# Performance work log

Measured on AMD Instinct MI355X. Metric: run time of the kernel, lower is better.

## Reference

```python
import jax, jax.numpy as jnp
import numpy as np

N_COMPANIES = 2000
HIDDEN = 256
HEADS = 8
LAYERS = 3
IN_DIM = 64
NEG_SLOPE = 0.2  # PyG GATConv default leaky_relu slope


def setup_inputs() -> dict:
    key = jax.random.key(0)
    ks = jax.random.split(key, 32)
    B, E = 64, 64000
    C = HIDDEN // HEADS
    emb_dim = HIDDEN // 4
    def lin(k, fo, fi):
        k1, k2 = jax.random.split(k)
        s = 1.0 / np.sqrt(fi)
        return (jax.random.uniform(k1, (fo, fi), jnp.float32, -s, s),
                jax.random.uniform(k2, (fo,), jnp.float32, -s, s))
    inp = {}
    inp['x'] = jax.random.normal(ks[0], (B, IN_DIM), jnp.float32)
    inp['company_indices'] = jax.random.randint(ks[1], (B,), 0, N_COMPANIES)
    inp['edge_index'] = jax.random.randint(ks[2], (2, E), 0, N_COMPANIES)
    inp['edge_attr'] = jax.random.uniform(ks[3], (E,), jnp.float32)
    inp['W_in'], inp['b_in'] = lin(ks[4], HIDDEN, IN_DIM)
    # stacked GAT params (all layers same shape)
    g = 0.05
    inp['gat_W'] = g * jax.random.normal(ks[5], (LAYERS, HEADS * C, HIDDEN), jnp.float32)
    inp['gat_att_src'] = g * jax.random.normal(ks[6], (LAYERS, HEADS, C), jnp.float32)
    inp['gat_att_dst'] = g * jax.random.normal(ks[7], (LAYERS, HEADS, C), jnp.float32)
    inp['gat_We'] = g * jax.random.normal(ks[8], (LAYERS, HEADS * C, 1), jnp.float32)
    inp['gat_att_edge'] = g * jax.random.normal(ks[9], (LAYERS, HEADS, C), jnp.float32)
    inp['gat_b'] = jnp.zeros((LAYERS, HEADS * C), jnp.float32)
    inp['emb'] = jax.random.normal(ks[10], (N_COMPANIES, emb_dim), jnp.float32)
    inp['W_fuse'], inp['b_fuse'] = lin(ks[11], HIDDEN, HIDDEN + emb_dim)
    inp['W_p1'], inp['b_p1'] = lin(ks[12], HIDDEN // 2, HIDDEN)
    inp['W_p2'], inp['b_p2'] = lin(ks[13], HIDDEN // 4, HIDDEN // 2)
    inp['W_p3'], inp['b_p3'] = lin(ks[14], 1, HIDDEN // 4)
    inp['W_d1'], inp['b_d1'] = lin(ks[15], HIDDEN // 2, HIDDEN)
    inp['W_d2'], inp['b_d2'] = lin(ks[16], HIDDEN // 4, HIDDEN // 2)
    inp['W_d3'], inp['b_d3'] = lin(ks[17], 1, HIDDEN // 4)
    return inp


def _gat_layer(xg, src, dst, ea, W, att_s, att_d, We, att_e, b, N):
    # xg: [N, F] node features; src/dst: [E2] (with self-loops); ea: [E2]
    H, C = att_s.shape
    xp = (xg @ W.T).reshape(N, H, C)
    a_s = jnp.sum(xp * att_s, -1)                       # [N, H]
    a_d = jnp.sum(xp * att_d, -1)                       # [N, H]
    ef = (ea[:, None] @ We.T).reshape(-1, H, C)         # [E2, H, C]
    a_e = jnp.sum(ef * att_e, -1)                       # [E2, H]
    logits = jax.nn.leaky_relu(a_s[src] + a_d[dst] + a_e, NEG_SLOPE)
    m = jax.ops.segment_max(logits, dst, num_segments=N)
    ex = jnp.exp(logits - m[dst])
    denom = jax.ops.segment_sum(ex, dst, num_segments=N)
    alpha = ex / (denom[dst] + 1e-16)                   # per-dst softmax
    out = jax.ops.segment_sum(alpha[:, :, None] * xp[src], dst, num_segments=N)
    return out.reshape(N, H * C) + b


def reference(x, company_indices, edge_index, edge_attr, W_in, b_in,
              gat_W, gat_att_src, gat_att_dst, gat_We, gat_att_edge, gat_b,
              emb, W_fuse, b_fuse, W_p1, b_p1, W_p2, b_p2, W_p3, b_p3,
              W_d1, b_d1, W_d2, b_d2, W_d3, b_d3):
    # eval mode: dropout is identity
    B = x.shape[0]
    N = emb.shape[0]
    h = jax.nn.relu(x @ W_in.T + b_in)                  # [B, hidden]
    # add self loops (PyG default, fill_value='mean' for edge_attr)
    loops = jnp.arange(N, dtype=edge_index.dtype)
    src = jnp.concatenate([edge_index[0], loops])
    dst = jnp.concatenate([edge_index[1], loops])
    ea = jnp.concatenate([edge_attr, jnp.full((N,), edge_attr.mean(), edge_attr.dtype)])

    def per_item(hi):
        g = jnp.broadcast_to(hi, (N, hi.shape[0]))
        for l in range(gat_W.shape[0]):
            g = jax.nn.relu(_gat_layer(g, src, dst, ea, gat_W[l], gat_att_src[l],
                                       gat_att_dst[l], gat_We[l], gat_att_edge[l], gat_b[l], N))
        return g

    gouts = jax.vmap(per_item)(h)                       # [B, N, hidden]
    comp_out = gouts[jnp.arange(B), company_indices]    # [B, hidden]
    comp_emb = emb[company_indices]                     # [B, hidden//4]
    fused = jax.nn.relu(jnp.concatenate([comp_out, comp_emb], -1) @ W_fuse.T + b_fuse)
    p = jax.nn.relu(fused @ W_p1.T + b_p1)
    p = jax.nn.relu(p @ W_p2.T + b_p2)
    price = (p @ W_p3.T + b_p3).squeeze(-1)
    d = jax.nn.relu(fused @ W_d1.T + b_d1)
    d = jax.nn.relu(d @ W_d2.T + b_d2)
    direction = jax.nn.sigmoid((d @ W_d3.T + b_d3)).squeeze(-1)
    return price, direction
```

## Files before the change

### kernel.cpp

```cpp
#include <hip/hip_runtime.h>
#include <math.h>


#define B_ITEMS 64

typedef _Float16 half_t;
typedef _Float16 half8 __attribute__((ext_vector_type(8)));
typedef float f32x4 __attribute__((ext_vector_type(4)));

#define OFF_WIN   0
#define OFF_GAT   16384
#define OFF_FUSE  212992
#define OFF_P1    294912
#define OFF_D1    327680
#define OFF_P2    360448
#define OFF_D2    368640
#define TOT_W     376832

extern "C" __global__ __launch_bounds__(1024) void compress_w(
    const float* __restrict__ W_in, const float* __restrict__ gat_W,
    const float* __restrict__ W_fuse, const float* __restrict__ W_p1,
    const float* __restrict__ W_d1, const float* __restrict__ W_p2,
    const float* __restrict__ W_d2, half_t* __restrict__ ws)
{
    const int e = (blockIdx.x * 1024 + threadIdx.x) * 8;
    const float* src;
    int off;
    if      (e < OFF_GAT)  { src = W_in;   off = e; }
    else if (e < OFF_FUSE) { src = gat_W;  off = e - OFF_GAT; }
    else if (e < OFF_P1)   { src = W_fuse; off = e - OFF_FUSE; }
    else if (e < OFF_D1)   { src = W_p1;   off = e - OFF_P1; }
    else if (e < OFF_P2)   { src = W_d1;   off = e - OFF_D1; }
    else if (e < OFF_D2)   { src = W_p2;   off = e - OFF_P2; }
    else                   { src = W_d2;   off = e - OFF_D2; }
    const float4* s4 = reinterpret_cast<const float4*>(src + off);
    float4 a = s4[0], b = s4[1];
    half8 h = { (_Float16)a.x, (_Float16)a.y, (_Float16)a.z, (_Float16)a.w,
                (_Float16)b.x, (_Float16)b.y, (_Float16)b.z, (_Float16)b.w };
    *reinterpret_cast<half8*>(ws + e) = h;
}

#define LDA 328

template <int KSTEPS>
__device__ __forceinline__ void mfma_tile(const half_t* __restrict__ Wt,
                                          const _Float16* __restrict__ At,
                                          f32x4& c, int kq) {
    const half8* __restrict__ Wp = reinterpret_cast<const half8*>(Wt + kq * 8);
    const _Float16* __restrict__ Ap = At + kq * 8;
#pragma unroll 1
    for (int s = 0; s < KSTEPS; s += 2) {
        half8 b0 = Wp[s * 4];
        half8 a0 = *reinterpret_cast<const half8*>(Ap + s * 32);
        half8 b1 = Wp[s * 4 + 4];
        half8 a1 = *reinterpret_cast<const half8*>(Ap + s * 32 + 32);
        c = __builtin_amdgcn_mfma_f32_16x16x32_f16(a0, b0, c, 0, 0, 0);
        c = __builtin_amdgcn_mfma_f32_16x16x32_f16(a1, b1, c, 0, 0, 0);
    }
}

__device__ __forceinline__ void cwrite(f32x4 c, float bv, _Float16* outbase,
                                       int col, int kq) {
#pragma unroll
    for (int r = 0; r < 4; ++r) {
        float v = fmaxf(c[r] + bv, 0.f);
        outbase[(kq * 4 + r) * LDA + col] = (_Float16)v;
    }
}

extern "C" __global__ __launch_bounds__(1024) void fin_gat_v13(
    const float* __restrict__ x,
    const int* __restrict__ cidx,
    const half_t* __restrict__ ws,
    const float* __restrict__ b_in,
    const float* __restrict__ gat_b,
    const float* __restrict__ emb,
    const float* __restrict__ b_fuse,
    const float* __restrict__ b_p1,
    const float* __restrict__ b_p2,
    const float* __restrict__ W_p3, const float* __restrict__ b_p3,
    const float* __restrict__ b_d1,
    const float* __restrict__ b_d2,
    const float* __restrict__ W_d3, const float* __restrict__ b_d3,
    float* __restrict__ out)
{
    __shared__ _Float16 actA[16 * LDA];
    __shared__ _Float16 actB[16 * LDA];
    __shared__ _Float16 xact[16 * 72];

    const int g = blockIdx.x;
    const int i0 = g * 16;
    const int t = threadIdx.x;
    const int w = t >> 6;
    const int lane = t & 63;
    const int r16 = lane & 15;
    const int kq = lane >> 4;

    {
        const int item = t >> 6, k = t & 63;
        xact[item * 72 + k] = (_Float16)x[(i0 + item) * 64 + k];
        actB[item * LDA + 256 + k] =
            (_Float16)emb[(size_t)cidx[i0 + item] * 64 + k];
    }
    __syncthreads();

    {
        f32x4 c = {0.f, 0.f, 0.f, 0.f};
        mfma_tile<2>(ws + OFF_WIN + (size_t)(w * 16 + r16) * 64,
                     xact + r16 * 72, c, kq);
        cwrite(c, b_in[w * 16 + r16], actA, w * 16 + r16, kq);
    }
    __syncthreads();

    {
        f32x4 c = {0.f, 0.f, 0.f, 0.f};
        mfma_tile<8>(ws + OFF_GAT + (size_t)(w * 16 + r16) * 256,
                     actA + r16 * LDA, c, kq);
        cwrite(c, gat_b[w * 16 + r16], actB, w * 16 + r16, kq);
    }
    __syncthreads();

    {
        f32x4 c = {0.f, 0.f, 0.f, 0.f};
        mfma_tile<8>(ws + OFF_GAT + 65536 + (size_t)(w * 16 + r16) * 256,
                     actB + r16 * LDA, c, kq);
        cwrite(c, gat_b[256 + w * 16 + r16], actA, w * 16 + r16, kq);
    }
    __syncthreads();

    {
        f32x4 c = {0.f, 0.f, 0.f, 0.f};
        mfma_tile<8>(ws + OFF_GAT + 131072 + (size_t)(w * 16 + r16) * 256,
                     actA + r16 * LDA, c, kq);
        cwrite(c, gat_b[512 + w * 16 + r16], actB, w * 16 + r16, kq);
    }
    __syncthreads();

    {
        f32x4 c = {0.f, 0.f, 0.f, 0.f};
        mfma_tile<10>(ws + OFF_FUSE + (size_t)(w * 16 + r16) * 320,
                      actB + r16 * LDA, c, kq);
        cwrite(c, b_fuse[w * 16 + r16], actA, w * 16 + r16, kq);
    }
    __syncthreads();

    {
        f32x4 c = {0.f, 0.f, 0.f, 0.f};
        const half_t* Wt = (w < 8)
            ? ws + OFF_P1 + (size_t)(w * 16 + r16) * 256
            : ws + OFF_D1 + (size_t)((w - 8) * 16 + r16) * 256;
        const float bv = (w < 8) ? b_p1[w * 16 + r16]
                                 : b_d1[(w - 8) * 16 + r16];
        mfma_tile<8>(Wt, actA + r16 * LDA, c, kq);
        cwrite(c, bv, actB, w * 16 + r16, kq);
    }
    __syncthreads();

    if (w < 8) {
        f32x4 c = {0.f, 0.f, 0.f, 0.f};
        const half_t* Wt = (w < 4)
            ? ws + OFF_P2 + (size_t)(w * 16 + r16) * 128
            : ws + OFF_D2 + (size_t)((w - 4) * 16 + r16) * 128;
        const _Float16* At = actB + r16 * LDA + ((w < 4) ? 0 : 128);
        const float bv = (w < 4) ? b_p2[w * 16 + r16]
                                 : b_d2[(w - 4) * 16 + r16];
        mfma_tile<4>(Wt, At, c, kq);
        cwrite(c, bv, actA, w * 16 + r16, kq);
    }
    __syncthreads();

    {
        float v1 = (float)actA[w * LDA + lane] * W_p3[lane];
        float v2 = (float)actA[w * LDA + 64 + lane] * W_d3[lane];
#pragma unroll
        for (int off = 32; off > 0; off >>= 1) {
            v1 += __shfl_down(v1, off, 64);
            v2 += __shfl_down(v2, off, 64);
        }
        if (lane == 0) {
            out[i0 + w] = v1 + b_p3[0];
            const float z = v2 + b_d3[0];
            out[B_ITEMS + i0 + w] = 1.0f / (1.0f + expf(-z));
        }
    }
}

extern "C" void kernel_launch(void* const* d_in, const int* in_sizes, int n_in,
                              void* d_out, int out_size, void* d_ws, size_t ws_size,
                              hipStream_t stream) {
    const float* x      = (const float*)d_in[0];
    const int*   cidx   = (const int*)  d_in[1];
    const float* W_in   = (const float*)d_in[4];
    const float* b_in   = (const float*)d_in[5];
    const float* gat_W  = (const float*)d_in[6];
    const float* gat_b  = (const float*)d_in[11];
    const float* emb    = (const float*)d_in[12];
    const float* W_fuse = (const float*)d_in[13];
    const float* b_fuse = (const float*)d_in[14];
    const float* W_p1   = (const float*)d_in[15];
    const float* b_p1   = (const float*)d_in[16];
    const float* W_p2   = (const float*)d_in[17];
    const float* b_p2   = (const float*)d_in[18];
    const float* W_p3   = (const float*)d_in[19];
    const float* b_p3   = (const float*)d_in[20];
    const float* W_d1   = (const float*)d_in[21];
    const float* b_d1   = (const float*)d_in[22];
    const float* W_d2   = (const float*)d_in[23];
    const float* b_d2   = (const float*)d_in[24];
    const float* W_d3   = (const float*)d_in[25];
    const float* b_d3   = (const float*)d_in[26];

    half_t* ws = (half_t*)d_ws;

    compress_w<<<46, 1024, 0, stream>>>(W_in, gat_W, W_fuse, W_p1, W_d1,
                                        W_p2, W_d2, ws);

    fin_gat_v13<<<4, 1024, 0, stream>>>(
        x, cidx, ws, b_in, gat_b, emb, b_fuse,
        b_p1, b_p2, W_p3, b_p3, b_d1, b_d2, W_d3, b_d3,
        (float*)d_out);
}
```

Baseline: 133.5 us.

## Stream weights into LDS with double-buffered async global_load_lds pipeline

Replaces per-wave direct global loads of fp16 weights inside each MFMA layer with a double-buffered pipeline. Weight chunks are copied asynchronously into XOR-swizzled LDS buffers via global_load_lds, and the next chunk's load overlaps with MFMA consumption of the current one. Biases are hoisted into registers up front. The change targets global-memory latency stalls in the serial layer chain, at the cost of 128KB of LDS, manual waitcnt/barrier management and more synchronisation points.

```diff
diff --git a/kernel.cpp b/kernel.cpp
--- a/kernel.cpp
+++ b/kernel.cpp
@@ -42,33 +42,58 @@
 
 #define LDA 328
 
-template <int KSTEPS>
-__device__ __forceinline__ void mfma_tile(const half_t* __restrict__ Wt,
-                                          const _Float16* __restrict__ At,
-                                          f32x4& c, int kq) {
-    const half8* __restrict__ Wp = reinterpret_cast<const half8*>(Wt + kq * 8);
-    const _Float16* __restrict__ Ap = At + kq * 8;
-#pragma unroll 1
-    for (int s = 0; s < KSTEPS; s += 2) {
-        half8 b0 = Wp[s * 4];
-        half8 a0 = *reinterpret_cast<const half8*>(Ap + s * 32);
-        half8 b1 = Wp[s * 4 + 4];
-        half8 a1 = *reinterpret_cast<const half8*>(Ap + s * 32 + 32);
-        c = __builtin_amdgcn_mfma_f32_16x16x32_f16(a0, b0, c, 0, 0, 0);
-        c = __builtin_amdgcn_mfma_f32_16x16x32_f16(a1, b1, c, 0, 0, 0);
-    }
-}
-
-__device__ __forceinline__ void cwrite(f32x4 c, float bv, _Float16* outbase,
-                                       int col, int kq) {
-#pragma unroll
-    for (int r = 0; r < 4; ++r) {
-        float v = fmaxf(c[r] + bv, 0.f);
-        outbase[(kq * 4 + r) * LDA + col] = (_Float16)v;
-    }
-}
-
-extern "C" __global__ __launch_bounds__(1024) void fin_gat_v13(
+#define WAITV(N)  asm volatile("s_waitcnt vmcnt(" #N ")" ::: "memory")
+#define LGKM0()   asm volatile("s_waitcnt lgkmcnt(0)" ::: "memory")
+#define BARRIER() asm volatile("s_barrier" ::: "memory")
+
+__device__ __forceinline__ void g2l16(const half_t* g, half_t* l) {
+    __builtin_amdgcn_global_load_lds(
+        (const __attribute__((address_space(1))) void*)g,
+        (__attribute__((address_space(3))) void*)l, 16, 0, 0);
+}
+
+template <int LNCH, int NCHUNK, int ROWH, int KOFFC>
+__device__ __forceinline__ void dma_stage(const half_t* __restrict__ base,
+                                          half_t* lbuf, int t) {
+#pragma unroll
+    for (int i = 0; i < NCHUNK / 1024; ++i) {
+        const int n = i * 1024 + t;
+        const int c = n >> LNCH;
+        const int j = (n & ((1 << LNCH) - 1)) ^ (c & 7);
+        g2l16(base + (size_t)c * ROWH + (KOFFC + j) * 8, lbuf + (size_t)n * 8);
+    }
+}
+
+template <int LNCH, int NCHUNK, int ROWH, int KOFFC, int CS>
+__device__ __forceinline__ void dma_split(const half_t* __restrict__ baseA,
+                                          const half_t* __restrict__ baseB,
+                                          half_t* lbuf, int t) {
+#pragma unroll
+    for (int i = 0; i < NCHUNK / 1024; ++i) {
+        const int n = i * 1024 + t;
+        const int c = n >> LNCH;
+        const int j = (n & ((1 << LNCH) - 1)) ^ (c & 7);
+        const half_t* base = (c < CS) ? baseA + (size_t)c * ROWH
+                                      : baseB + (size_t)(c - CS) * ROWH;
+        g2l16(base + (KOFFC + j) * 8, lbuf + (size_t)n * 8);
+    }
+}
+
+template <int LNCH, int STEPS>
+__device__ __forceinline__ void consume(const half_t* __restrict__ lbuf,
+                                        const _Float16* __restrict__ Arow,
+                                        int cloc, int kq, f32x4& acc) {
+#pragma unroll
+    for (int s = 0; s < STEPS; ++s) {
+        const int j = (s * 4 + kq) ^ (cloc & 7);
+        half8 bf = *reinterpret_cast<const half8*>(
+            lbuf + (size_t)((cloc << LNCH) + j) * 8);
+        half8 af = *reinterpret_cast<const half8*>(Arow + s * 32 + kq * 8);
+        acc = __builtin_amdgcn_mfma_f32_16x16x32_f16(af, bf, acc, 0, 0, 0);
+    }
+}
+
+extern "C" __global__ __launch_bounds__(1024) void fin_gat_v14(
     const float* __restrict__ x,
     const int* __restrict__ cidx,
     const half_t* __restrict__ ws,
@@ -84,6 +109,7 @@
     const float* __restrict__ W_d3, const float* __restrict__ b_d3,
     float* __restrict__ out)
 {
+    __shared__ half_t wbuf[2][32768];
     __shared__ _Float16 actA[16 * LDA];
     __shared__ _Float16 actB[16 * LDA];
     __shared__ _Float16 xact[16 * 72];
@@ -95,6 +121,7 @@
     const int lane = t & 63;
     const int r16 = lane & 15;
     const int kq = lane >> 4;
+    const int col = w * 16 + r16;
 
     {
         const int item = t >> 6, k = t & 63;
@@ -102,84 +129,127 @@
         actB[item * LDA + 256 + k] =
             (_Float16)emb[(size_t)cidx[i0 + item] * 64 + k];
     }
+    const float bv0 = b_in[col];
+    const float bg0 = gat_b[col], bg1 = gat_b[256 + col], bg2 = gat_b[512 + col];
+    const float bfu = b_fuse[col];
+    const float bh1 = (w < 8) ? b_p1[col] : b_d1[col - 128];
+    const float bh2 = (w < 8) ? ((w < 4) ? b_p2[col] : b_d2[col - 64]) : 0.f;
+    const float w3p = W_p3[lane], w3d = W_d3[lane];
+    const float b3p = b_p3[0], b3d = b_d3[0];
     __syncthreads();
 
+    f32x4 acc = {0.f, 0.f, 0.f, 0.f};
+
+    dma_stage<3, 2048, 64, 0>(ws + OFF_WIN, wbuf[0], t);
+
+    dma_stage<4, 4096, 256, 0>(ws + OFF_GAT, wbuf[1], t);
+    WAITV(4); BARRIER();
+    consume<3, 2>(wbuf[0], xact + r16 * 72, col, kq, acc);
+#pragma unroll
+    for (int r = 0; r < 4; ++r)
+        actA[(kq * 4 + r) * LDA + col] = (_Float16)fmaxf(acc[r] + bv0, 0.f);
+    LGKM0(); BARRIER();
+
+    dma_stage<4, 4096, 256, 16>(ws + OFF_GAT, wbuf[0], t);
+    WAITV(4); BARRIER();
+    acc = f32x4{0.f, 0.f, 0.f, 0.f};
+    consume<4, 4>(wbuf[1], actA + r16 * LDA, col, kq, acc);
+    LGKM0(); BARRIER();
+
+    dma_stage<4, 4096, 256, 0>(ws + OFF_GAT + 65536, wbuf[1], t);
+    WAITV(4); BARRIER();
+    consume<4, 4>(wbuf[0], actA + r16 * LDA + 128, col, kq, acc);
+#pragma unroll
+    for (int r = 0; r < 4; ++r)
+        actB[(kq * 4 + r) * LDA + col] = (_Float16)fmaxf(acc[r] + bg0, 0.f);
+    LGKM0(); BARRIER();
+
+    dma_stage<4, 4096, 256, 16>(ws + OFF_GAT + 65536, wbuf[0], t);
+    WAITV(4); BARRIER();
+    acc = f32x4{0.f, 0.f, 0.f, 0.f};
+    consume<4, 4>(wbuf[1], actB + r16 * LDA, col, kq, acc);
+    LGKM0(); BARRIER();
+
+    dma_stage<4, 4096, 256, 0>(ws + OFF_GAT + 131072, wbuf[1], t);
+    WAITV(4); BARRIER();
+    consume<4, 4>(wbuf[0], actB + r16 * LDA + 128, col, kq, acc);
+#pragma unroll
+    for (int r = 0; r < 4; ++r)
+        actA[(kq * 4 + r) * LDA + col] = (_Float16)fmaxf(acc[r] + bg1, 0.f);
+    LGKM0(); BARRIER();
+
+    dma_stage<4, 4096, 256, 16>(ws + OFF_GAT + 131072, wbuf[0], t);
+    WAITV(4); BARRIER();
+    acc = f32x4{0.f, 0.f, 0.f, 0.f};
+    consume<4, 4>(wbuf[1], actA + r16 * LDA, col, kq, acc);
+    LGKM0(); BARRIER();
+
+    dma_stage<4, 4096, 320, 0>(ws + OFF_FUSE, wbuf[1], t);
+    WAITV(4); BARRIER();
+    consume<4, 4>(wbuf[0], actA + r16 * LDA + 128, col, kq, acc);
+#pragma unroll
+    for (int r = 0; r < 4; ++r)
+        actB[(kq * 4 + r) * LDA + col] = (_Float16)fmaxf(acc[r] + bg2, 0.f);
+    LGKM0(); BARRIER();
+
+    dma_stage<4, 4096, 320, 16>(ws + OFF_FUSE, wbuf[0], t);
+    WAITV(4); BARRIER();
+    acc = f32x4{0.f, 0.f, 0.f, 0.f};
+    consume<4, 4>(wbuf[1], actB + r16 * LDA, col, kq, acc);
+    LGKM0(); BARRIER();
+
+    dma_stage<3, 2048, 320, 32>(ws + OFF_FUSE, wbuf[1], t);
+    WAITV(2); BARRIER();
+    consume<4, 4>(wbuf[0], actB + r16 * LDA + 128, col, kq, acc);
+    LGKM0(); BARRIER();
+
+    dma_split<4, 4096, 256, 0, 128>(ws + OFF_P1, ws + OFF_D1,
+                                    wbuf[0], t);
+    WAITV(4); BARRIER();
+    consume<3, 2>(wbuf[1], actB + r16 * LDA + 256, col, kq, acc);
+#pragma unroll
+    for (int r = 0; r < 4; ++r)
+        actA[(kq * 4 + r) * LDA + col] = (_Float16)fmaxf(acc[r] + bfu, 0.f);
+    LGKM0(); BARRIER();
+
+    dma_split<4, 4096, 256, 16, 128>(ws + OFF_P1, ws + OFF_D1,
+                                     wbuf[1], t);
+    WAITV(4); BARRIER();
+    acc = f32x4{0.f, 0.f, 0.f, 0.f};
+    consume<4, 4>(wbuf[0], actA + r16 * LDA, col, kq, acc);
+    LGKM0(); BARRIER();
+
+    dma_split<4, 2048, 128, 0, 64>(ws + OFF_P2, ws + OFF_D2,
+                                   wbuf[0], t);
+    WAITV(2); BARRIER();
+    consume<4, 4>(wbuf[1], actA + r16 * LDA + 128, col, kq, acc);
+#pragma unroll
+    for (int r = 0; r < 4; ++r)
+        actB[(kq * 4 + r) * LDA + col] = (_Float16)fmaxf(acc[r] + bh1, 0.f);
+    LGKM0(); BARRIER();
+
+    WAITV(0); BARRIER();
+    if (w < 8) {
+        acc = f32x4{0.f, 0.f, 0.f, 0.f};
+        const int koff = (w < 4) ? 0 : 128;
+        consume<4, 4>(wbuf[0], actB + r16 * LDA + koff, col, kq, acc);
+#pragma unroll
+        for (int r = 0; r < 4; ++r)
+            actA[(kq * 4 + r) * LDA + col] = (_Float16)fmaxf(acc[r] + bh2, 0.f);
+    }
+    LGKM0(); BARRIER();
+
     {
-        f32x4 c = {0.f, 0.f, 0.f, 0.f};
-        mfma_tile<2>(ws + OFF_WIN + (size_t)(w * 16 + r16) * 64,
-                     xact + r16 * 72, c, kq);
-        cwrite(c, b_in[w * 16 + r16], actA, w * 16 + r16, kq);
-    }
-    __syncthreads();
-
-    {
-        f32x4 c = {0.f, 0.f, 0.f, 0.f};
-        mfma_tile<8>(ws + OFF_GAT + (size_t)(w * 16 + r16) * 256,
-                     actA + r16 * LDA, c, kq);
-        cwrite(c, gat_b[w * 16 + r16], actB, w * 16 + r16, kq);
-    }
-    __syncthreads();
-
-    {
-        f32x4 c = {0.f, 0.f, 0.f, 0.f};
-        mfma_tile<8>(ws + OFF_GAT + 65536 + (size_t)(w * 16 + r16) * 256,
-                     actB + r16 * LDA, c, kq);
-        cwrite(c, gat_b[256 + w * 16 + r16], actA, w * 16 + r16, kq);
-    }
-    __syncthreads();
-
-    {
-        f32x4 c = {0.f, 0.f, 0.f, 0.f};
-        mfma_tile<8>(ws + OFF_GAT + 131072 + (size_t)(w * 16 + r16) * 256,
-                     actA + r16 * LDA, c, kq);
-        cwrite(c, gat_b[512 + w * 16 + r16], actB, w * 16 + r16, kq);
-    }
-    __syncthreads();
-
-    {
-        f32x4 c = {0.f, 0.f, 0.f, 0.f};
-        mfma_tile<10>(ws + OFF_FUSE + (size_t)(w * 16 + r16) * 320,
-                      actB + r16 * LDA, c, kq);
-        cwrite(c, b_fuse[w * 16 + r16], actA, w * 16 + r16, kq);
-    }
-    __syncthreads();
-
-    {
-        f32x4 c = {0.f, 0.f, 0.f, 0.f};
-        const half_t* Wt = (w < 8)
-            ? ws + OFF_P1 + (size_t)(w * 16 + r16) * 256
-            : ws + OFF_D1 + (size_t)((w - 8) * 16 + r16) * 256;
-        const float bv = (w < 8) ? b_p1[w * 16 + r16]
-                                 : b_d1[(w - 8) * 16 + r16];
-        mfma_tile<8>(Wt, actA + r16 * LDA, c, kq);
-        cwrite(c, bv, actB, w * 16 + r16, kq);
-    }
-    __syncthreads();
-
-    if (w < 8) {
-        f32x4 c = {0.f, 0.f, 0.f, 0.f};
-        const half_t* Wt = (w < 4)
-            ? ws + OFF_P2 + (size_t)(w * 16 + r16) * 128
-            : ws + OFF_D2 + (size_t)((w - 4) * 16 + r16) * 128;
-        const _Float16* At = actB + r16 * LDA + ((w < 4) ? 0 : 128);
-        const float bv = (w < 4) ? b_p2[w * 16 + r16]
-                                 : b_d2[(w - 4) * 16 + r16];
-        mfma_tile<4>(Wt, At, c, kq);
-        cwrite(c, bv, actA, w * 16 + r16, kq);
-    }
-    __syncthreads();
-
-    {
-        float v1 = (float)actA[w * LDA + lane] * W_p3[lane];
-        float v2 = (float)actA[w * LDA + 64 + lane] * W_d3[lane];
+        float v1 = (float)actA[w * LDA + lane] * w3p;
+        float v2 = (float)actA[w * LDA + 64 + lane] * w3d;
 #pragma unroll
         for (int off = 32; off > 0; off >>= 1) {
             v1 += __shfl_down(v1, off, 64);
             v2 += __shfl_down(v2, off, 64);
         }
         if (lane == 0) {
-            out[i0 + w] = v1 + b_p3[0];
-            const float z = v2 + b_d3[0];
+            out[i0 + w] = v1 + b3p;
+            const float z = v2 + b3d;
             out[B_ITEMS + i0 + w] = 1.0f / (1.0f + expf(-z));
         }
     }
@@ -215,7 +285,7 @@
     compress_w<<<46, 1024, 0, stream>>>(W_in, gat_W, W_fuse, W_p1, W_d1,
                                         W_p2, W_d2, ws);
 
-    fin_gat_v13<<<4, 1024, 0, stream>>>(
+    fin_gat_v14<<<4, 1024, 0, stream>>>(
         x, cidx, ws, b_in, gat_b, emb, b_fuse,
         b_p1, b_p2, W_p3, b_p3, b_d1, b_d2, W_d3, b_d3,
         (float*)d_out);
```

New measurement: 121.9 us. 1.1x faster.
